# Kernel tuning notes

Hardware: AMD Instinct MI355X
Metric: run time of the kernel (lower is better)

The kernel has to match this reference:

```python
import jax, jax.numpy as jnp
import numpy as np

EPS = 1e-5
SELECT_NUM = 10   # hard-coded in Support_AUG_Image
NEIGHBOR_K = 3
SEMI_K = 3


def _conv(x, w):
    return jax.lax.conv_general_dilated(x, w, (1, 1), 'SAME',
                                        dimension_numbers=('NCHW', 'OIHW', 'NCHW'))


def _bn(x, g, b):
    # BatchNorm2d, training mode: biased batch stats over (N, H, W)
    mu = jnp.mean(x, (0, 2, 3), keepdims=True)
    var = jnp.mean((x - mu) ** 2, (0, 2, 3), keepdims=True)
    return g[None, :, None, None] * (x - mu) * jax.lax.rsqrt(var + EPS) + b[None, :, None, None]


def _lrelu(x):
    return jnp.where(x >= 0, x, 0.2 * x)


def _pool(x):
    return jax.lax.reduce_window(x, -jnp.inf, jax.lax.max,
                                 (1, 1, 2, 2), (1, 1, 2, 2), 'VALID')


def _features(x, params):
    # conv-bn-lrelu-pool, conv-bn-lrelu-pool, conv-bn-lrelu, conv-bn-lrelu
    for i, (w, g, b) in enumerate(params):
        x = _lrelu(_bn(_conv(x, w), g, b))
        if i < 2:
            x = _pool(x)
    return x  # [N, 64, 21, 21] for 84x84 input


def _descriptors(feat):
    # [B, C, h, w] -> [B, h*w, C], rows L2-normalized (query local descriptors)
    B, C = feat.shape[0], feat.shape[1]
    d = feat.reshape(B, C, -1).transpose(0, 2, 1)
    return d / jnp.sqrt(jnp.sum(d * d, -1, keepdims=True))


def _col_normalize(s):
    # [C, m]: L2-normalize each column (support descriptor)
    return s / jnp.sqrt(jnp.sum(s * s, 0, keepdims=True))


def _img2class_sim(q_desc, S, k):
    # q_desc [B, n, C] row-normalized; S [K, C, m] raw support banks.
    # Per class (K small, fixed): cosine sims [B, n, m], top-k over m, sum.
    sims = []
    for j in range(S.shape[0]):
        inner = q_desc @ _col_normalize(S[j])          # [B, n, m]
        tv = jax.lax.top_k(inner, k)[0]                # [B, n, k]
        sims.append(jnp.sum(tv, axis=(1, 2)))
    return jnp.stack(sims, 1)                          # [B, K]


def _forward(input1, input2, input3, params):
    K, shot = input2.shape[0], input2.shape[1]
    q = _features(input1, params)                      # [Bq, 64, 21, 21]
    sup = _features(input2.reshape((-1,) + input2.shape[2:]), params)
    C, h, w = sup.shape[1], sup.shape[2], sup.shape[3]
    # per class: permute(1,0,2,3).view(C,-1) -> [K, C, shot*h*w]
    S = sup.reshape(K, shot, C, h, w).transpose(0, 2, 1, 3, 4).reshape(K, C, shot * h * w)
    u = _features(input3, params)                      # [Bu, 64, 21, 21]

    # Support_AUG_Image: similarity of unlabeled pool vs support, softmax over classes,
    # then append top-10 unlabeled feature maps (raw) to each class bank.
    u_desc = _descriptors(u)
    sim_u = jax.nn.softmax(_img2class_sim(u_desc, S, SEMI_K), axis=1)  # [Bu, K]
    aug = []
    for j in range(K):
        idx = jax.lax.top_k(sim_u[:, j], SELECT_NUM)[1]                # [10]
        sel = u[idx].transpose(1, 0, 2, 3).reshape(C, -1)              # [C, 10*h*w]
        aug.append(jnp.concatenate([S[j], sel], axis=1))
    S_aug = jnp.stack(aug, 0)                          # [K, C, shot*h*w + 10*h*w]

    # ImgtoClass_Metric on queries vs augmented support
    q_desc = _descriptors(q)
    return _img2class_sim(q_desc, S_aug, NEIGHBOR_K)   # [Bq, K]


def setup_inputs() -> dict:
    key = jax.random.key(0)
    ks = jax.random.split(key, 8)
    inp = {
        'input1': jax.random.normal(ks[0], (75, 3, 84, 84), jnp.float32),
        'input2': jax.random.normal(ks[1], (5, 5, 3, 84, 84), jnp.float32),
        'input3': jax.random.normal(ks[2], (64, 3, 84, 84), jnp.float32),
        'w1': jax.random.normal(ks[3], (64, 3, 3, 3), jnp.float32) * 0.1,
        'w2': jax.random.normal(ks[4], (64, 64, 3, 3), jnp.float32) * 0.05,
        'w3': jax.random.normal(ks[5], (64, 64, 3, 3), jnp.float32) * 0.05,
        'w4': jax.random.normal(ks[6], (64, 64, 3, 3), jnp.float32) * 0.05,
    }
    for i in (1, 2, 3, 4):
        inp[f'g{i}'] = jnp.ones((64,), jnp.float32)
        inp[f'b{i}'] = jnp.zeros((64,), jnp.float32)
    return inp


def reference(input1, input2, input3, w1, g1, b1, w2, g2, b2, w3, g3, b3, w4, g4, b4):
    params = [(w1, g1, b1), (w2, g2, b2), (w3, g3, b3), (w4, g4, b4)]
    return _forward(input1, input2, input3, params)
```

## Files before the change

kernel.cpp:

```cpp
#include <hip/hip_runtime.h>
#include <hip/hip_bf16.h>
#include <math.h>

typedef __hip_bfloat16 bf16;
typedef __attribute__((ext_vector_type(8))) short short8;
typedef __attribute__((ext_vector_type(4))) float floatx4;
typedef __attribute__((ext_vector_type(4))) unsigned short ushort4v;

#define LRELU(v) ((v) < 0.f ? 0.2f * (v) : (v))

__device__ __forceinline__ float b2f(bf16 x) { return __bfloat162float(x); }
__device__ __forceinline__ int img_group(int n) { return n < 75 ? 0 : (n < 100 ? 1 : 2); }

__global__ __launch_bounds__(64) void detect_kernel(
    const void* in1, const void* in2, const void* in3,
    const void* w1, const void* w2, const void* w3, const void* w4,
    const void* g1, const void* g2, const void* g3, const void* g4,
    int* __restrict__ flags)
{
  int t = threadIdx.x;
  if (t >= 11) return;
  const void* p = nullptr; int nh = 384, isg = 0;
  switch (t) {
    case 0: p = in1; break;  case 1: p = in2; break;  case 2: p = in3; break;
    case 3: p = w1;  break;  case 4: p = w2;  break;  case 5: p = w3;  break;
    case 6: p = w4;  break;
    case 7: p = g1; nh = 64; isg = 1; break;
    case 8: p = g2; nh = 64; isg = 1; break;
    case 9: p = g3; nh = 64; isg = 1; break;
    case 10: p = g4; nh = 64; isg = 1; break;
  }
  const unsigned short* h = (const unsigned short*)p;
  int cnt = 0;
  for (int i = 0; i < nh; ++i) {
    unsigned short v = h[i];
    if (isg) {
      if (v == 0) ++cnt;
    } else {
      int e = (v >> 7) & 0xFF;
      if (e >= 160 || (e > 0 && e <= 80)) ++cnt;
    }
  }
  flags[t] = isg ? (cnt >= 16) : (cnt >= 48);
}

#define ZT0 167280
#define ZT1 1972592
#define ZT2 2896240
#define ZT3 3819888
#define ZT4 4565104
__device__ __forceinline__ void border_yx(int b, int W, int* y, int* x) {
  if (b < W) { *y = 0; *x = b; }
  else if (b < 2 * W) { *y = W - 1; *x = b - W; }
  else { int cc = b - 2 * W; *y = 1 + (cc >> 1); *x = (cc & 1) ? (W - 1) : 0; }
}
__global__ __launch_bounds__(256) void zero_pads(
    bf16* __restrict__ imgp, bf16* __restrict__ p1t,
    bf16* __restrict__ p2t, bf16* __restrict__ f3t, bf16* __restrict__ descAll)
{
  int i = blockIdx.x * 256 + threadIdx.x;
  bf16 z = __float2bfloat16(0.f);
  if (i < ZT0) {
    int plane = i / 340, b = i % 340;
    int y, x; border_yx(b, 86, &y, &x);
    imgp[((size_t)plane * 86 + y) * 86 + x] = z;
  } else if (i < ZT1) {
    int r = i - ZT0;
    int img = r / (172 * 64); r %= 172 * 64;
    int colb = r >> 6, ch = r & 63;
    int y, x; border_yx(colb, 44, &y, &x);
    p1t[(((size_t)img * 1936) + y * 44 + x) * 64 + ch] = z;
  } else if (i < ZT2) {
    int r = i - ZT1;
    int img = r / (88 * 64); r %= 88 * 64;
    int colb = r >> 6, ch = r & 63;
    int y, x; border_yx(colb, 23, &y, &x);
    p2t[(((size_t)img * 529) + y * 23 + x) * 64 + ch] = z;
  } else if (i < ZT3) {
    int r = i - ZT2;
    int img = r / (88 * 64); r %= 88 * 64;
    int colb = r >> 6, ch = r & 63;
    int y, x; border_yx(colb, 23, &y, &x);
    f3t[(((size_t)img * 529) + y * 23 + x) * 64 + ch] = z;
  } else if (i < ZT4) {
    int r = i - ZT3;
    int img = r / (71 * 64); r %= 71 * 64;
    int row = 441 + (r >> 6), ch = r & 63;
    descAll[((size_t)img * 512 + row) * 64 + ch] = z;
  }
}

#define NIMG 3471552
#define BIMG 13562
#define NWP  110592
#define BWP  432
#define BW1  8
#define BGB  2
#define NPART (4 * 164 * 128)
#define NZ (NPART + 320 + 375)
#define BZ  331
__global__ __launch_bounds__(256) void setup_all(
    const void* in1, const void* in2, const void* in3,
    const void* w1, const void* w2, const void* w3, const void* w4,
    const void* g1, const void* b1, const void* g2, const void* b2,
    const void* g3, const void* b3, const void* g4, const void* b4,
    const int* __restrict__ flags,
    bf16* __restrict__ imgp, bf16* __restrict__ w1p,
    bf16* __restrict__ wp2, bf16* __restrict__ wp3, bf16* __restrict__ wp4,
    float* __restrict__ gb, float* __restrict__ part,
    float* __restrict__ uscore, float* __restrict__ qscore)
{
  int b = blockIdx.x;
  if (b < BIMG) {
    int k = b * 256 + threadIdx.x;
    if (k >= NIMG) return;
    const void* src; int idx, f;
    if (k < 75 * 21168)       { src = in1; idx = k;               f = flags[0]; }
    else if (k < 100 * 21168) { src = in2; idx = k - 75 * 21168;  f = flags[1]; }
    else                      { src = in3; idx = k - 100 * 21168; f = flags[2]; }
    bf16 v = f ? __float2bfloat16(((const float*)src)[idx]) : ((const bf16*)src)[idx];
    int n = k / 21168, r = k % 21168;
    int ci = r / 7056, pix = r % 7056;
    int y = pix / 84, x = pix % 84;
    imgp[((size_t)(n * 3 + ci) * 86 + y + 1) * 86 + x + 1] = v;
  } else if (b < BIMG + BWP) {
    int idx = (b - BIMG) * 256 + threadIdx.x;
    if (idx >= NWP) return;
    int which = idx / 36864, i = idx % 36864;
    const void* src = which == 0 ? w2 : (which == 1 ? w3 : w4);
    bf16* dst = which == 0 ? wp2 : (which == 1 ? wp3 : wp4);
    int f = flags[4 + which];
    float v = f ? ((const float*)src)[i] : b2f(((const bf16*)src)[i]);
    int co = i / 576, ci = (i / 9) % 64, tap = i % 9;
    dst[((size_t)tap * 64 + co) * 64 + ci] = __float2bfloat16(v);
  } else if (b < BIMG + BWP + BW1) {
    int i = (b - BIMG - BWP) * 256 + threadIdx.x;
    if (i >= 2048) return;
    int co = i >> 5, k = i & 31;
    float v = 0.f;
    if (k < 27) {
      int f = flags[3];
      v = f ? ((const float*)w1)[co * 27 + k] : b2f(((const bf16*)w1)[co * 27 + k]);
    }
    w1p[i] = __float2bfloat16(v);
  } else if (b < BIMG + BWP + BW1 + BGB) {
    int i = (b - BIMG - BWP - BW1) * 256 + threadIdx.x;
    if (i >= 512) return;
    int which = i >> 6, cc = i & 63;
    const void* s;
    switch (which) {
      case 0: s = g1; break; case 1: s = b1; break;
      case 2: s = g2; break; case 3: s = b2; break;
      case 4: s = g3; break; case 5: s = b3; break;
      case 6: s = g4; break; default: s = b4; break;
    }
    int isg = !(which & 1);
    int f = isg ? flags[7 + (which >> 1)] : 0;
    gb[i] = f ? ((const float*)s)[cc] : b2f(((const bf16*)s)[cc]);
  } else {
    int i = (b - BIMG - BWP - BW1 - BGB) * 256 + threadIdx.x;
    if (i < NPART) part[i] = 0.f;
    else if (i < NPART + 320) uscore[i - NPART] = 0.f;
    else if (i < NZ) qscore[i - NPART - 320] = 0.f;
  }
}

__global__ __launch_bounds__(256) void conv1_stats_mfma(
    const bf16* __restrict__ imgp, const bf16* __restrict__ w1p,
    float* __restrict__ part)
{
  __shared__ float sacc[128];
  int n = blockIdx.x, tile = blockIdx.y;
  int lane = threadIdx.x & 63;
  int q = lane >> 4, c = lane & 15;
  int wave = threadIdx.x >> 6;
  const short* ib = (const short*)(imgp + (size_t)n * 3 * 86 * 86);
  short8 B[4];
  #pragma unroll
  for (int j4 = 0; j4 < 4; ++j4) {
    int p = tile * 256 + j4 * 64 + wave * 16 + c;
    bool valid = p < 7056;
    int pc = valid ? p : 0;
    int y = pc / 84, x = pc % 84;
    short bs[8];
    #pragma unroll
    for (int j = 0; j < 8; ++j) {
      int k = q * 8 + j;
      int ci = k / 9, tap = k - ci * 9;
      int dy = tap / 3, dx = tap - dy * 3;
      bs[j] = (k < 27 && valid) ? ib[(ci * 86 + y + dy) * 86 + x + dx] : (short)0;
    }
    B[j4] = (short8){bs[0], bs[1], bs[2], bs[3], bs[4], bs[5], bs[6], bs[7]};
  }
  float s[16], sq[16];
  #pragma unroll
  for (int t = 0; t < 4; ++t) {
    const short* ap = (const short*)w1p + (t * 16 + c) * 32 + q * 8;
    short8 A = *(const short8*)ap;
    floatx4 a0 = {0.f,0.f,0.f,0.f}, a1 = a0, a2 = a0, a3 = a0;
    a0 = __builtin_amdgcn_mfma_f32_16x16x32_bf16(A, B[0], a0, 0, 0, 0);
    a1 = __builtin_amdgcn_mfma_f32_16x16x32_bf16(A, B[1], a1, 0, 0, 0);
    a2 = __builtin_amdgcn_mfma_f32_16x16x32_bf16(A, B[2], a2, 0, 0, 0);
    a3 = __builtin_amdgcn_mfma_f32_16x16x32_bf16(A, B[3], a3, 0, 0, 0);
    #pragma unroll
    for (int r = 0; r < 4; ++r) {
      s[t * 4 + r]  = a0[r] + a1[r] + a2[r] + a3[r];
      sq[t * 4 + r] = fmaf(a0[r], a0[r], fmaf(a1[r], a1[r],
                      fmaf(a2[r], a2[r], a3[r] * a3[r])));
    }
  }
  #pragma unroll
  for (int off = 1; off < 16; off <<= 1)
    #pragma unroll
    for (int i = 0; i < 16; ++i) {
      s[i]  += __shfl_xor(s[i], off);
      sq[i] += __shfl_xor(sq[i], off);
    }
  if (threadIdx.x < 128) sacc[threadIdx.x] = 0.f;
  __syncthreads();
  if (c == 0) {
    #pragma unroll
    for (int t = 0; t < 4; ++t)
      #pragma unroll
      for (int r = 0; r < 4; ++r) {
        int co = t * 16 + q * 4 + r;
        atomicAdd(&sacc[co], s[t * 4 + r]);
        atomicAdd(&sacc[64 + co], sq[t * 4 + r]);
      }
  }
  __syncthreads();
  if (threadIdx.x < 128) atomicAdd(&part[n * 128 + threadIdx.x], sacc[threadIdx.x]);
}

__global__ __launch_bounds__(256) void finalize_kernel(
    const float* __restrict__ part, const float* __restrict__ gam, const float* __restrict__ bet,
    float* __restrict__ scl, float* __restrict__ sht, float HWf)
{
  int t = threadIdx.x;
  if (t >= 192) return;
  int g = t / 64, c = t % 64;
  const int starts[3] = {0, 75, 100}, cnts[3] = {75, 25, 64};
  float S = 0.f, Q = 0.f;
  for (int im = starts[g]; im < starts[g] + cnts[g]; ++im) {
    S += part[im * 128 + c];
    Q += part[im * 128 + 64 + c];
  }
  float N = (float)cnts[g] * HWf;
  float mean = S / N;
  float var = fmaxf(Q / N - mean * mean, 0.f);
  float rstd = rsqrtf(var + 1e-5f);
  float sc = gam[c] * rstd;
  scl[t] = sc;
  sht[t] = bet[c] - mean * sc;
}

__global__ __launch_bounds__(256) void conv1_pool_mfma(
    const bf16* __restrict__ imgp, const bf16* __restrict__ w1p,
    const float* __restrict__ scl, const float* __restrict__ sht,
    bf16* __restrict__ p1t)
{
  int n = blockIdx.x, tile = blockIdx.y;
  int lane = threadIdx.x & 63, wave = threadIdx.x >> 6;
  int q = lane >> 4, c = lane & 15;
  int pp = tile * 64 + wave * 16 + c;
  bool valid = pp < 1764;
  int pc = valid ? pp : 0;
  int py = pc / 42, px = pc % 42;
  int g = img_group(n);
  const short* ib = (const short*)(imgp + (size_t)n * 3 * 86 * 86);
  short8 B[4];
  #pragma unroll
  for (int quad = 0; quad < 4; ++quad) {
    int y = 2 * py + (quad >> 1), x = 2 * px + (quad & 1);
    short bs[8];
    #pragma unroll
    for (int j = 0; j < 8; ++j) {
      int k = q * 8 + j;
      int ci = k / 9, tap = k - ci * 9;
      int dy = tap / 3, dx = tap - dy * 3;
      bs[j] = (k < 27) ? ib[(ci * 86 + y + dy) * 86 + x + dx] : (short)0;
    }
    B[quad] = (short8){bs[0], bs[1], bs[2], bs[3], bs[4], bs[5], bs[6], bs[7]};
  }
  bf16* ob = p1t + ((size_t)n * 1936 + (py + 1) * 44 + px + 1) * 64;
  #pragma unroll
  for (int t = 0; t < 4; ++t) {
    const short* ap = (const short*)w1p + (t * 16 + c) * 32 + q * 8;
    short8 A = *(const short8*)ap;
    floatx4 a0 = {0.f,0.f,0.f,0.f}, a1 = a0, a2 = a0, a3 = a0;
    a0 = __builtin_amdgcn_mfma_f32_16x16x32_bf16(A, B[0], a0, 0, 0, 0);
    a1 = __builtin_amdgcn_mfma_f32_16x16x32_bf16(A, B[1], a1, 0, 0, 0);
    a2 = __builtin_amdgcn_mfma_f32_16x16x32_bf16(A, B[2], a2, 0, 0, 0);
    a3 = __builtin_amdgcn_mfma_f32_16x16x32_bf16(A, B[3], a3, 0, 0, 0);
    if (valid) {
      ushort4v st;
      #pragma unroll
      for (int r = 0; r < 4; ++r) {
        int co = t * 16 + q * 4 + r;
        float sc_ = scl[g * 64 + co], sh_ = sht[g * 64 + co];
        float v0 = a0[r] * sc_ + sh_; v0 = LRELU(v0);
        float v1 = a1[r] * sc_ + sh_; v1 = LRELU(v1);
        float v2 = a2[r] * sc_ + sh_; v2 = LRELU(v2);
        float v3 = a3[r] * sc_ + sh_; v3 = LRELU(v3);
        float best = fmaxf(fmaxf(v0, v1), fmaxf(v2, v3));
        bf16 bv = __float2bfloat16(best);
        st[r] = *(unsigned short*)&bv;
      }
      *(ushort4v*)(ob + t * 16 + q * 4) = st;
    }
  }
}

__global__ __launch_bounds__(256) void bnt_kernel(
    const float* __restrict__ in, const float* __restrict__ scl, const float* __restrict__ sht,
    bf16* __restrict__ outp, int HW, int W, int PW, int PHPW)
{
  __shared__ bf16 tile[64][65];
  int n = blockIdx.x, t0 = blockIdx.y * 64;
  int g = img_group(n);
  for (int idx = threadIdx.x; idx < 4096; idx += 256) {
    int ci = idx >> 6, pix = idx & 63;
    int p = t0 + pix;
    float v = 0.f;
    if (p < HW) {
      v = in[((size_t)n * 64 + ci) * HW + p] * scl[g * 64 + ci] + sht[g * 64 + ci];
      v = LRELU(v);
    }
    tile[pix][ci] = __float2bfloat16(v);
  }
  __syncthreads();
  for (int idx = threadIdx.x; idx < 4096; idx += 256) {
    int pix = idx >> 6, ci = idx & 63;
    int p = t0 + pix;
    if (p < HW) {
      int y = p / W, x = p % W;
      outp[((size_t)n * PHPW + (y + 1) * PW + (x + 1)) * 64 + ci] = tile[pix][ci];
    }
  }
}

__global__ __launch_bounds__(256) void conv_mfma_kernel(
    const bf16* __restrict__ in_t, const bf16* __restrict__ wp,
    void* __restrict__ outp, int HW, int W, int PW, int PHPW, int out_is_f32,
    float* __restrict__ part)
{
  __shared__ float sacc[128];
  if (threadIdx.x < 128) sacc[threadIdx.x] = 0.f;
  __syncthreads();
  int n = blockIdx.x, tile = blockIdx.y;
  int wave = threadIdx.x >> 6, lane = threadIdx.x & 63;
  int q = lane >> 4, c = lane & 15;
  int p = tile * 64 + wave * 16 + c;
  bool valid = p < HW;
  int pc = valid ? p : HW - 1;
  int y = pc / W, x = pc % W;
  const bf16* ibase = in_t + ((size_t)n * PHPW + y * PW + x) * 64;

  short8 B0[9], B1[9];
  #pragma unroll
  for (int dy = 0; dy < 3; ++dy)
    #pragma unroll
    for (int dx = 0; dx < 3; ++dx) {
      const short* bp = (const short*)(ibase + (dy * PW + dx) * 64) + q * 8;
      B0[dy * 3 + dx] = *(const short8*)bp;
      B1[dy * 3 + dx] = *(const short8*)(bp + 32);
    }

  for (int t = 0; t < 4; ++t) {
    floatx4 acc = {0.f, 0.f, 0.f, 0.f};
    #pragma unroll
    for (int tap = 0; tap < 9; ++tap) {
      const short* ap = (const short*)(wp + ((size_t)tap * 64 + t * 16 + c) * 64) + q * 8;
      short8 A0 = *(const short8*)ap;
      short8 A1 = *(const short8*)(ap + 32);
      acc = __builtin_amdgcn_mfma_f32_16x16x32_bf16(A0, B0[tap], acc, 0, 0, 0);
      acc = __builtin_amdgcn_mfma_f32_16x16x32_bf16(A1, B1[tap], acc, 0, 0, 0);
    }
    float sv[4], qv[4];
    #pragma unroll
    for (int r = 0; r < 4; ++r) {
      float v = valid ? acc[r] : 0.f;
      sv[r] = v; qv[r] = v * v;
    }
    #pragma unroll
    for (int off = 1; off < 16; off <<= 1)
      #pragma unroll
      for (int r = 0; r < 4; ++r) {
        sv[r] += __shfl_xor(sv[r], off);
        qv[r] += __shfl_xor(qv[r], off);
      }
    if (c == 0) {
      #pragma unroll
      for (int r = 0; r < 4; ++r) {
        int co = t * 16 + q * 4 + r;
        atomicAdd(&sacc[co], sv[r]);
        atomicAdd(&sacc[64 + co], qv[r]);
      }
    }
    if (valid) {
      #pragma unroll
      for (int r = 0; r < 4; ++r) {
        int co = t * 16 + q * 4 + r;
        size_t oidx = ((size_t)n * 64 + co) * HW + p;
        if (out_is_f32) ((float*)outp)[oidx] = acc[r];
        else ((bf16*)outp)[oidx] = __float2bfloat16(acc[r]);
      }
    }
  }
  __syncthreads();
  if (threadIdx.x < 128) atomicAdd(&part[n * 128 + threadIdx.x], sacc[threadIdx.x]);
}

__global__ __launch_bounds__(256) void bn2_pool_t(
    const bf16* __restrict__ c2, const float* __restrict__ scl, const float* __restrict__ sht,
    bf16* __restrict__ p2t)
{
  __shared__ bf16 tile[64][65];
  int n = blockIdx.x, t0 = blockIdx.y * 64;
  int g = img_group(n);
  for (int idx = threadIdx.x; idx < 4096; idx += 256) {
    int co = idx >> 6, pix = idx & 63;
    int p = t0 + pix;
    bf16 outv = __float2bfloat16(0.f);
    if (p < 441) {
      float sc = scl[g * 64 + co], sh = sht[g * 64 + co];
      int py = p / 21, px = p % 21;
      const bf16* base = c2 + ((size_t)n * 64 + co) * 1764;
      float best = -1e30f;
      #pragma unroll
      for (int dy = 0; dy < 2; ++dy)
        #pragma unroll
        for (int dx = 0; dx < 2; ++dx) {
          float v = b2f(base[(2 * py + dy) * 42 + 2 * px + dx]) * sc + sh;
          v = LRELU(v);
          best = fmaxf(best, v);
        }
      outv = __float2bfloat16(best);
    }
    tile[pix][co] = outv;
  }
  __syncthreads();
  for (int idx = threadIdx.x; idx < 4096; idx += 256) {
    int pix = idx >> 6, co = idx & 63;
    int p = t0 + pix;
    if (p < 441) {
      int y = p / 21, x = p % 21;
      p2t[((size_t)n * 529 + (y + 1) * 23 + x + 1) * 64 + co] = tile[pix][co];
    }
  }
}

__global__ __launch_bounds__(256) void bn_norm_desc(
    const float* __restrict__ feat, const float* __restrict__ scl, const float* __restrict__ sht,
    bf16* __restrict__ descAll)
{
  __shared__ float tile[64][65];
  int n = blockIdx.x, t0 = blockIdx.y * 64;
  int g = img_group(n);
  for (int idx = threadIdx.x; idx < 4096; idx += 256) {
    int ci = idx >> 6, pix = idx & 63;
    int p = t0 + pix;
    float v = 0.f;
    if (p < 441) {
      v = feat[((size_t)n * 64 + ci) * 441 + p] * scl[g * 64 + ci] + sht[g * 64 + ci];
      v = LRELU(v);
    }
    tile[pix][ci] = v;
  }
  __syncthreads();
  int pix = threadIdx.x >> 2, quar = threadIdx.x & 3;
  float ss = 0.f;
  #pragma unroll
  for (int c = 0; c < 16; ++c) { float v = tile[pix][quar * 16 + c]; ss += v * v; }
  ss += __shfl_xor(ss, 1);
  ss += __shfl_xor(ss, 2);
  int p = t0 + pix;
  float inv = (p < 441) ? rsqrtf(ss) : 0.f;
  bf16* o = descAll + ((size_t)n * 512 + p) * 64 + quar * 16;
  #pragma unroll
  for (int c = 0; c < 16; ++c) o[c] = __float2bfloat16(tile[pix][quar * 16 + c] * inv);
}

__global__ __launch_bounds__(256) void sbank_copy(
    const bf16* __restrict__ descAll, bf16* __restrict__ SnT)
{
  int j = blockIdx.x / 9, chunk = blockIdx.x % 9;
  int col = chunk * 256 + threadIdx.x;
  short* o = (short*)(SnT + ((size_t)j * 2304 + col) * 64);
  if (col < 2205) {
    int shot = col / 441, pos = col % 441;
    const short* s = (const short*)(descAll + ((size_t)(75 + j * 5 + shot) * 512 + pos) * 64);
    #pragma unroll
    for (int k = 0; k < 8; ++k) *(short8*)(o + k * 8) = *(const short8*)(s + k * 8);
  } else {
    short8 z = {0,0,0,0,0,0,0,0};
    #pragma unroll
    for (int k = 0; k < 8; ++k) *(short8*)(o + k * 8) = z;
  }
}

__global__ __launch_bounds__(256) void saug_copy(
    const bf16* __restrict__ descAll, const bf16* __restrict__ SnT,
    const int* __restrict__ sel, bf16* __restrict__ SaT)
{
  int j = blockIdx.x / 26, chunk = blockIdx.x % 26;
  int col = chunk * 256 + threadIdx.x;
  short* o = (short*)(SaT + ((size_t)j * 6656 + col) * 64);
  const short* s;
  if (col < 2205) {
    s = (const short*)(SnT + ((size_t)j * 2304 + col) * 64);
  } else if (col < 6615) {
    int rel = col - 2205;
    int i = rel / 441, pos = rel % 441;
    int img = 100 + sel[j * 10 + i];
    s = (const short*)(descAll + ((size_t)img * 512 + pos) * 64);
  } else {
    short8 z = {0,0,0,0,0,0,0,0};
    #pragma unroll
    for (int k = 0; k < 8; ++k) *(short8*)(o + k * 8) = z;
    return;
  }
  #pragma unroll
  for (int k = 0; k < 8; ++k) *(short8*)(o + k * 8) = *(const short8*)(s + k * 8);
}

#define SIM_NS 4
#define SIM_CH 128
__global__ __launch_bounds__(256) void sim_mfma_kernel(
    const bf16* __restrict__ desc, const bf16* __restrict__ bankT,
    float* __restrict__ partial, int m, int mp, int NI)
{
  __shared__ short lds[2][SIM_CH * 72];
  int nblk = (int)gridDim.x;
  int qq = nblk >> 3;
  int wg = (blockIdx.x & 7) * qq + (blockIdx.x >> 3);
  int img = wg % NI;
  int t_ = wg / NI;
  int cls = t_ % 5;
  int z = t_ / 5;
  int slice = z & (SIM_NS - 1);
  int rg = z >> 2;
  int tid = threadIdx.x;
  int wave = tid >> 6, lane = tid & 63;
  int q = lane >> 4, c = lane & 15;
  int R = rg * 256 + wave * 64;
  bool wactive = R < 441;

  const short* dp = (const short*)(desc + ((size_t)img * 512 + R + c) * 64) + q * 8;
  short8 b0l = *(const short8*)dp;          short8 b0h = *(const short8*)(dp + 32);
  short8 b1l = *(const short8*)(dp + 1024); short8 b1h = *(const short8*)(dp + 1056);
  short8 b2l = *(const short8*)(dp + 2048); short8 b2h = *(const short8*)(dp + 2080);
  short8 b3l = *(const short8*)(dp + 3072); short8 b3h = *(const short8*)(dp + 3104);

  float t0[4], t1[4], t2[4];
  #pragma unroll
  for (int i = 0; i < 4; ++i) { t0[i] = -1e4f; t1[i] = -1e4f; t2[i] = -1e4f; }

  const floatx4 z4 = {0.f, 0.f, 0.f, 0.f};

  const short* bankc = (const short*)(bankT + (size_t)cls * mp * 64);
  int NC = mp / SIM_CH;
  int ch0 = (slice * NC) / SIM_NS, ch1 = ((slice + 1) * NC) / SIM_NS;
  int nfull = m >> 4;

  {
    const short* src = bankc + (size_t)ch0 * (SIM_CH * 64);
    #pragma unroll
    for (int k = 0; k < 4; ++k) {
      int s = tid + k * 256;
      *(short8*)(&lds[0][(s >> 3) * 72 + (s & 7) * 8]) = *(const short8*)(src + (size_t)s * 8);
    }
  }
  __syncthreads();

  for (int ch = ch0; ch < ch1; ++ch) {
    int cur = (ch - ch0) & 1;
    bool havenext = (ch + 1 < ch1);
    short8 rA, rB, rC, rD;
    if (havenext) {
      const short* src = bankc + (size_t)(ch + 1) * (SIM_CH * 64);
      rA = *(const short8*)(src + (size_t)tid * 8);
      rB = *(const short8*)(src + (size_t)(tid + 256) * 8);
      rC = *(const short8*)(src + (size_t)(tid + 512) * 8);
      rD = *(const short8*)(src + (size_t)(tid + 768) * 8);
    }
    if (wactive) {
      #pragma unroll
      for (int t = 0; t < 8; ++t) {
        const short* lp = &lds[cur][(t * 16 + c) * 72 + q * 8];
        short8 A0 = *(const short8*)lp;
        short8 A1 = *(const short8*)(lp + 32);
        floatx4 a0 = __builtin_amdgcn_mfma_f32_16x16x32_bf16(A0, b0l, z4, 0, 0, 0);
        floatx4 a1 = __builtin_amdgcn_mfma_f32_16x16x32_bf16(A0, b1l, z4, 0, 0, 0);
        floatx4 a2 = __builtin_amdgcn_mfma_f32_16x16x32_bf16(A0, b2l, z4, 0, 0, 0);
        floatx4 a3 = __builtin_amdgcn_mfma_f32_16x16x32_bf16(A0, b3l, z4, 0, 0, 0);
        a0 = __builtin_amdgcn_mfma_f32_16x16x32_bf16(A1, b0h, a0, 0, 0, 0);
        a1 = __builtin_amdgcn_mfma_f32_16x16x32_bf16(A1, b1h, a1, 0, 0, 0);
        a2 = __builtin_amdgcn_mfma_f32_16x16x32_bf16(A1, b2h, a2, 0, 0, 0);
        a3 = __builtin_amdgcn_mfma_f32_16x16x32_bf16(A1, b3h, a3, 0, 0, 0);
        int gt = ch * 8 + t;
        if (gt < nfull) {
          #pragma unroll
          for (int r = 0; r < 4; ++r) {
            float v0 = a0[r];
            t2[0] = __builtin_amdgcn_fmed3f(v0, t2[0], t1[0]);
            t1[0] = __builtin_amdgcn_fmed3f(v0, t1[0], t0[0]);
            t0[0] = fmaxf(t0[0], v0);
            float v1 = a1[r];
            t2[1] = __builtin_amdgcn_fmed3f(v1, t2[1], t1[1]);
            t1[1] = __builtin_amdgcn_fmed3f(v1, t1[1], t0[1]);
            t0[1] = fmaxf(t0[1], v1);
            float v2 = a2[r];
            t2[2] = __builtin_amdgcn_fmed3f(v2, t2[2], t1[2]);
            t1[2] = __builtin_amdgcn_fmed3f(v2, t1[2], t0[2]);
            t0[2] = fmaxf(t0[2], v2);
            float v3 = a3[r];
            t2[3] = __builtin_amdgcn_fmed3f(v3, t2[3], t1[3]);
            t1[3] = __builtin_amdgcn_fmed3f(v3, t1[3], t0[3]);
            t0[3] = fmaxf(t0[3], v3);
          }
        } else {
          #pragma unroll
          for (int r = 0; r < 4; ++r) {
            bool colok = (gt * 16 + q * 4 + r) < m;
            float v0 = colok ? a0[r] : -1e4f;
            t2[0] = __builtin_amdgcn_fmed3f(v0, t2[0], t1[0]);
            t1[0] = __builtin_amdgcn_fmed3f(v0, t1[0], t0[0]);
            t0[0] = fmaxf(t0[0], v0);
            float v1 = colok ? a1[r] : -1e4f;
            t2[1] = __builtin_amdgcn_fmed3f(v1, t2[1], t1[1]);
            t1[1] = __builtin_amdgcn_fmed3f(v1, t1[1], t0[1]);
            t0[1] = fmaxf(t0[1], v1);
            float v2 = colok ? a2[r] : -1e4f;
            t2[2] = __builtin_amdgcn_fmed3f(v2, t2[2], t1[2]);
            t1[2] = __builtin_amdgcn_fmed3f(v2, t1[2], t0[2]);
            t0[2] = fmaxf(t0[2], v2);
            float v3 = colok ? a3[r] : -1e4f;
            t2[3] = __builtin_amdgcn_fmed3f(v3, t2[3], t1[3]);
            t1[3] = __builtin_amdgcn_fmed3f(v3, t1[3], t0[3]);
            t0[3] = fmaxf(t0[3], v3);
          }
        }
      }
    }
    if (havenext) {
      *(short8*)(&lds[cur ^ 1][(tid >> 3) * 72 + (tid & 7) * 8]) = rA;
      int s1 = tid + 256;
      *(short8*)(&lds[cur ^ 1][(s1 >> 3) * 72 + (s1 & 7) * 8]) = rB;
      int s2 = tid + 512;
      *(short8*)(&lds[cur ^ 1][(s2 >> 3) * 72 + (s2 & 7) * 8]) = rC;
      int s3 = tid + 768;
      *(short8*)(&lds[cur ^ 1][(s3 >> 3) * 72 + (s3 & 7) * 8]) = rD;
    }
    __syncthreads();
  }

  if (wactive) {
    #pragma unroll
    for (int off = 16; off < 64; off <<= 1) {
      #pragma unroll
      for (int i = 0; i < 4; ++i) {
        float b0v = __shfl_xor(t0[i], off);
        float b1v = __shfl_xor(t1[i], off);
        float b2v = __shfl_xor(t2[i], off);
        float n0 = fmaxf(t0[i], b0v);
        float n1 = fminf(fmaxf(t0[i], b1v), fmaxf(t1[i], b0v));
        float n2 = fminf(fminf(fmaxf(t0[i], b2v), fmaxf(t1[i], b1v)), fmaxf(t2[i], b0v));
        t0[i] = n0; t1[i] = n1; t2[i] = n2;
      }
    }
    if (q == 0) {
      size_t base = ((size_t)(img * 5 + cls) * SIM_NS + slice) * 512;
      #pragma unroll
      for (int i = 0; i < 4; ++i) {
        int row = R + i * 16 + c;
        if (row < 441) {
          floatx4 v = {t0[i], t1[i], t2[i], 0.f};
          *(floatx4*)(&partial[(base + row) * 4]) = v;
        }
      }
    }
  }
}

__global__ __launch_bounds__(256) void sim_merge_kernel(
    const float* __restrict__ partial, float* __restrict__ out)
{
  __shared__ float red[4];
  int ic = blockIdx.x;
  int tid = threadIdx.x;
  const floatx4* p0 = (const floatx4*)partial + (size_t)ic * SIM_NS * 512;
  float sum = 0.f;
  for (int row = tid; row < 441; row += 256) {
    floatx4 a = p0[row];
    float t0 = a[0], t1 = a[1], t2 = a[2];
    #pragma unroll
    for (int s = 1; s < SIM_NS; ++s) {
      floatx4 b = p0[s * 512 + row];
      float b0 = b[0], b1 = b[1], b2 = b[2];
      float n0 = fmaxf(t0, b0);
      float n1 = fminf(fmaxf(t0, b1), fmaxf(t1, b0));
      float n2 = fminf(fminf(fmaxf(t0, b2), fmaxf(t1, b1)), fmaxf(t2, b0));
      t0 = n0; t1 = n1; t2 = n2;
    }
    sum += t0 + t1 + t2;
  }
  #pragma unroll
  for (int off = 32; off > 0; off >>= 1) sum += __shfl_down(sum, off);
  int wv = tid >> 6;
  if ((tid & 63) == 0) red[wv] = sum;
  __syncthreads();
  if (tid == 0) out[ic] = red[0] + red[1] + red[2] + red[3];
}

__global__ __launch_bounds__(64) void softtop_kernel(
    const float* __restrict__ uscore, int* __restrict__ sel)
{
  __shared__ float simu[320];
  int i = threadIdx.x;
  {
    float v[5]; float mx = -1e30f;
    #pragma unroll
    for (int j = 0; j < 5; ++j) { v[j] = uscore[i * 5 + j]; mx = fmaxf(mx, v[j]); }
    float s = 0.f;
    #pragma unroll
    for (int j = 0; j < 5; ++j) { v[j] = expf(v[j] - mx); s += v[j]; }
    float inv = 1.f / s;
    #pragma unroll
    for (int j = 0; j < 5; ++j) simu[i * 5 + j] = v[j] * inv;
  }
  __syncthreads();
  if (i < 5) {
    unsigned long long mask = 0ull;
    for (int r = 0; r < 10; ++r) {
      float best = -1e30f; int bi = 0;
      for (int k = 0; k < 64; ++k) {
        if ((mask >> k) & 1ull) continue;
        float v = simu[k * 5 + i];
        if (v > best) { best = v; bi = k; }
      }
      mask |= (1ull << bi);
      sel[i * 10 + r] = bi;
    }
  }
}

__global__ __launch_bounds__(256) void outcvt_kernel(
    const float* __restrict__ qv, const int* __restrict__ flags, float* __restrict__ o)
{
  int i = blockIdx.x * 256 + threadIdx.x;
  if (i >= 375) return;
  float v = qv[i];
  int bad = (!isfinite(v)) || fabsf(v) > 2e3f;
  if (bad) {
    int code = flags[0] * 4 + flags[3] * 2 + flags[7];
    v = -(1e8f * (1.f + 0.01f * (float)code));
  }
  o[i] = v;
}

extern "C" void kernel_launch(void* const* d_in, const int* in_sizes, int n_in,
                              void* d_out, int out_size, void* d_ws, size_t ws_size,
                              hipStream_t stream) {
  const void* in1 = d_in[0];
  const void* in2 = d_in[1];
  const void* in3 = d_in[2];
  const void* w1  = d_in[3];
  const void* w2  = d_in[4];
  const void* w3  = d_in[5];
  const void* w4  = d_in[6];
  const void* g1  = d_in[7];
  const void* b1  = d_in[8];
  const void* g2  = d_in[9];
  const void* b2  = d_in[10];
  const void* g3  = d_in[11];
  const void* b3  = d_in[12];
  const void* g4  = d_in[13];
  const void* b4  = d_in[14];

  char* base = (char*)d_ws;
  size_t off = 0;
  auto alloc = [&](size_t bytes) -> void* {
    void* p = base + off;
    off += (bytes + 255) & ~(size_t)255;
    return p;
  };
  int*   flags = (int*)alloc(16 * 4);
  bf16*  wp2   = (bf16*)alloc(36864 * 2);
  bf16*  wp3   = (bf16*)alloc(36864 * 2);
  bf16*  wp4   = (bf16*)alloc(36864 * 2);
  bf16*  w1p   = (bf16*)alloc(2048 * 2);
  float* gb    = (float*)alloc(8 * 64 * 4);
  float* part  = (float*)alloc(4 * 164 * 128 * 4);
  float* scl1  = (float*)alloc(192 * 4);
  float* sht1  = (float*)alloc(192 * 4);
  float* scl2  = (float*)alloc(192 * 4);
  float* sht2  = (float*)alloc(192 * 4);
  float* scl3  = (float*)alloc(192 * 4);
  float* sht3  = (float*)alloc(192 * 4);
  float* scl4  = (float*)alloc(192 * 4);
  float* sht4  = (float*)alloc(192 * 4);
  float* uscore = (float*)alloc(320 * 4);
  int*   sel    = (int*)alloc(50 * 4);
  float* qscore = (float*)alloc(375 * 4);
  float* simpart = (float*)alloc((size_t)375 * SIM_NS * 512 * 4 * 4);
  bf16*  imgp = (bf16*)alloc((size_t)164 * 3 * 86 * 86 * 2);
  bf16*  p1t  = (bf16*)alloc((size_t)164 * 1936 * 64 * 2);
  bf16*  p2t  = (bf16*)alloc((size_t)164 * 529 * 64 * 2);
  bf16*  f3t  = (bf16*)alloc((size_t)164 * 529 * 64 * 2);
  bf16*  descAll = (bf16*)alloc((size_t)164 * 512 * 64 * 2);
  bf16*  conv2o   = (bf16*)alloc((size_t)164 * 64 * 1764 * 2);
  bf16* SnT     = (bf16*)alloc((size_t)5 * 2304 * 64 * 2);
  bf16* SaT     = (bf16*)alloc((size_t)5 * 6656 * 64 * 2);
  float* feat3 = (float*)p1t;
  float* feat4 = (float*)((char*)p1t + (size_t)164 * 64 * 441 * 4);
  float* part1 = part;
  float* part2 = part + 164 * 128;
  float* part3 = part + 2 * 164 * 128;
  float* part4 = part + 3 * 164 * 128;

  detect_kernel<<<1, 64, 0, stream>>>(in1, in2, in3, w1, w2, w3, w4, g1, g2, g3, g4, flags);
  zero_pads<<<(ZT4 + 255) / 256, 256, 0, stream>>>(imgp, p1t, p2t, f3t, descAll);
  setup_all<<<BIMG + BWP + BW1 + BGB + BZ, 256, 0, stream>>>(
      in1, in2, in3, w1, w2, w3, w4, g1, b1, g2, b2, g3, b3, g4, b4,
      flags, imgp, w1p, wp2, wp3, wp4, gb, part, uscore, qscore);

  conv1_stats_mfma<<<dim3(164, 28), 256, 0, stream>>>(imgp, w1p, part1);
  finalize_kernel<<<1, 256, 0, stream>>>(part1, gb + 0 * 64, gb + 1 * 64, scl1, sht1, 7056.f);
  conv1_pool_mfma<<<dim3(164, 28), 256, 0, stream>>>(imgp, w1p, scl1, sht1, p1t);

  conv_mfma_kernel<<<dim3(164, 28), 256, 0, stream>>>(p1t, wp2, conv2o, 1764, 42, 44, 1936, 0, part2);
  finalize_kernel<<<1, 256, 0, stream>>>(part2, gb + 2 * 64, gb + 3 * 64, scl2, sht2, 1764.f);
  bn2_pool_t<<<dim3(164, 7), 256, 0, stream>>>(conv2o, scl2, sht2, p2t);

  conv_mfma_kernel<<<dim3(164, 7), 256, 0, stream>>>(p2t, wp3, feat3, 441, 21, 23, 529, 1, part3);
  finalize_kernel<<<1, 256, 0, stream>>>(part3, gb + 4 * 64, gb + 5 * 64, scl3, sht3, 441.f);
  bnt_kernel<<<dim3(164, 7), 256, 0, stream>>>(feat3, scl3, sht3, f3t, 441, 21, 23, 529);

  conv_mfma_kernel<<<dim3(164, 7), 256, 0, stream>>>(f3t, wp4, feat4, 441, 21, 23, 529, 1, part4);
  finalize_kernel<<<1, 256, 0, stream>>>(part4, gb + 6 * 64, gb + 7 * 64, scl4, sht4, 441.f);

  bn_norm_desc<<<dim3(164, 7), 256, 0, stream>>>(feat4, scl4, sht4, descAll);
  sbank_copy<<<45, 256, 0, stream>>>(descAll, SnT);

  sim_mfma_kernel<<<64 * 5 * 2 * SIM_NS, 256, 0, stream>>>(descAll + (size_t)100 * 512 * 64, SnT, simpart, 2205, 2304, 64);
  sim_merge_kernel<<<320, 256, 0, stream>>>(simpart, uscore);
  softtop_kernel<<<1, 64, 0, stream>>>(uscore, sel);
  saug_copy<<<130, 256, 0, stream>>>(descAll, SnT, sel, SaT);

  sim_mfma_kernel<<<75 * 5 * 2 * SIM_NS, 256, 0, stream>>>(descAll, SaT, simpart, 6615, 6656, 75);
  sim_merge_kernel<<<375, 256, 0, stream>>>(simpart, qscore);
  outcvt_kernel<<<2, 256, 0, stream>>>(qscore, flags, (float*)d_out);
}
```

Before: 985.4 us.

## Split BN statistics out of conv kernels into separate row-reduction kernel

Removes the in-kernel batch-norm sum/sum-of-squares reduction (shuffles, LDS atomics, global atomics) from the MFMA conv kernel. The statistics are instead computed by a new rowstats kernel that re-reads each conv output row and reduces it with one wavefront per channel row. This trades atomic contention and extra conv-kernel work for an extra launch and a second full read of the conv outputs. It also makes the stats deterministic, since part is now written directly instead of accumulated atomically.

Result: no change. 992.9 us (+0.8%).

```diff
diff --git a/kernel.cpp b/kernel.cpp
--- a/kernel.cpp
+++ b/kernel.cpp
@@ -4,6 +4,7 @@
 
 typedef __hip_bfloat16 bf16;
 typedef __attribute__((ext_vector_type(8))) short short8;
+typedef __attribute__((ext_vector_type(4))) short short4v;
 typedef __attribute__((ext_vector_type(4))) float floatx4;
 typedef __attribute__((ext_vector_type(4))) unsigned short ushort4v;
 
@@ -232,6 +233,43 @@
   if (threadIdx.x < 128) atomicAdd(&part[n * 128 + threadIdx.x], sacc[threadIdx.x]);
 }
 
+__global__ __launch_bounds__(256) void rowstats_kernel(
+    const void* __restrict__ data, float* __restrict__ part, int HW, int is_f32)
+{
+  int row = blockIdx.x * 4 + (threadIdx.x >> 6);
+  int lane = threadIdx.x & 63;
+  int n = row >> 6, co = row & 63;
+  float S = 0.f, Q = 0.f;
+  if (is_f32) {
+    const float* p = (const float*)data + (size_t)row * HW;
+    for (int i = lane; i < HW; i += 64) {
+      float v = p[i];
+      S += v; Q = fmaf(v, v, Q);
+    }
+  } else {
+    const short* p = (const short*)data + (size_t)row * HW;
+    int ng = HW >> 2;
+    for (int i = lane; i < ng; i += 64) {
+      short4v v = *(const short4v*)(p + i * 4);
+      #pragma unroll
+      for (int j = 0; j < 4; ++j) {
+        unsigned short u = (unsigned short)v[j];
+        float f = __uint_as_float(((unsigned)u) << 16);
+        S += f; Q = fmaf(f, f, Q);
+      }
+    }
+  }
+  #pragma unroll
+  for (int off = 1; off < 64; off <<= 1) {
+    S += __shfl_xor(S, off);
+    Q += __shfl_xor(Q, off);
+  }
+  if (lane == 0) {
+    part[n * 128 + co] = S;
+    part[n * 128 + 64 + co] = Q;
+  }
+}
+
 __global__ __launch_bounds__(256) void finalize_kernel(
     const float* __restrict__ part, const float* __restrict__ gam, const float* __restrict__ bet,
     float* __restrict__ scl, float* __restrict__ sht, float HWf)
@@ -341,14 +379,10 @@
 
 __global__ __launch_bounds__(256) void conv_mfma_kernel(
     const bf16* __restrict__ in_t, const bf16* __restrict__ wp,
-    void* __restrict__ outp, int HW, int W, int PW, int PHPW, int out_is_f32,
-    float* __restrict__ part)
-{
-  __shared__ float sacc[128];
-  if (threadIdx.x < 128) sacc[threadIdx.x] = 0.f;
-  __syncthreads();
+    void* __restrict__ outp, int HW, int W, int PW, int PHPW, int out_is_f32)
+{
   int n = blockIdx.x, tile = blockIdx.y;
-  int wave = threadIdx.x >> 6, lane = threadIdx.x & 63;
+  int lane = threadIdx.x & 63, wave = threadIdx.x >> 6;
   int q = lane >> 4, c = lane & 15;
   int p = tile * 64 + wave * 16 + c;
   bool valid = p < HW;
@@ -375,27 +409,6 @@
       short8 A1 = *(const short8*)(ap + 32);
       acc = __builtin_amdgcn_mfma_f32_16x16x32_bf16(A0, B0[tap], acc, 0, 0, 0);
       acc = __builtin_amdgcn_mfma_f32_16x16x32_bf16(A1, B1[tap], acc, 0, 0, 0);
-    }
-    float sv[4], qv[4];
-    #pragma unroll
-    for (int r = 0; r < 4; ++r) {
-      float v = valid ? acc[r] : 0.f;
-      sv[r] = v; qv[r] = v * v;
-    }
-    #pragma unroll
-    for (int off = 1; off < 16; off <<= 1)
-      #pragma unroll
-      for (int r = 0; r < 4; ++r) {
-        sv[r] += __shfl_xor(sv[r], off);
-        qv[r] += __shfl_xor(qv[r], off);
-      }
-    if (c == 0) {
-      #pragma unroll
-      for (int r = 0; r < 4; ++r) {
-        int co = t * 16 + q * 4 + r;
-        atomicAdd(&sacc[co], sv[r]);
-        atomicAdd(&sacc[64 + co], qv[r]);
-      }
     }
     if (valid) {
       #pragma unroll
@@ -407,8 +420,6 @@
       }
     }
   }
-  __syncthreads();
-  if (threadIdx.x < 128) atomicAdd(&part[n * 128 + threadIdx.x], sacc[threadIdx.x]);
 }
 
 __global__ __launch_bounds__(256) void bn2_pool_t(
@@ -829,15 +840,18 @@
   finalize_kernel<<<1, 256, 0, stream>>>(part1, gb + 0 * 64, gb + 1 * 64, scl1, sht1, 7056.f);
   conv1_pool_mfma<<<dim3(164, 28), 256, 0, stream>>>(imgp, w1p, scl1, sht1, p1t);
 
-  conv_mfma_kernel<<<dim3(164, 28), 256, 0, stream>>>(p1t, wp2, conv2o, 1764, 42, 44, 1936, 0, part2);
+  conv_mfma_kernel<<<dim3(164, 28), 256, 0, stream>>>(p1t, wp2, conv2o, 1764, 42, 44, 1936, 0);
+  rowstats_kernel<<<2624, 256, 0, stream>>>(conv2o, part2, 1764, 0);
   finalize_kernel<<<1, 256, 0, stream>>>(part2, gb + 2 * 64, gb + 3 * 64, scl2, sht2, 1764.f);
   bn2_pool_t<<<dim3(164, 7), 256, 0, stream>>>(conv2o, scl2, sht2, p2t);
 
-  conv_mfma_kernel<<<dim3(164, 7), 256, 0, stream>>>(p2t, wp3, feat3, 441, 21, 23, 529, 1, part3);
+  conv_mfma_kernel<<<dim3(164, 7), 256, 0, stream>>>(p2t, wp3, feat3, 441, 21, 23, 529, 1);
+  rowstats_kernel<<<2624, 256, 0, stream>>>(feat3, part3, 441, 1);
   finalize_kernel<<<1, 256, 0, stream>>>(part3, gb + 4 * 64, gb + 5 * 64, scl3, sht3, 441.f);
   bnt_kernel<<<dim3(164, 7), 256, 0, stream>>>(feat3, scl3, sht3, f3t, 441, 21, 23, 529);
 
-  conv_mfma_kernel<<<dim3(164, 7), 256, 0, stream>>>(f3t, wp4, feat4, 441, 21, 23, 529, 1, part4);
+  conv_mfma_kernel<<<dim3(164, 7), 256, 0, stream>>>(f3t, wp4, feat4, 441, 21, 23, 529, 1);
+  rowstats_kernel<<<2624, 256, 0, stream>>>(feat4, part4, 441, 1);
   finalize_kernel<<<1, 256, 0, stream>>>(part4, gb + 6 * 64, gb + 7 * 64, scl4, sht4, 441.f);
 
   bn_norm_desc<<<dim3(164, 7), 256, 0, stream>>>(feat4, scl4, sht4, descAll);
```
